# Kernel optimization log

Measured on AMD Instinct MI355X. Metric: run time of the kernel, lower is better.

The kernel has to match this reference:

```python
import jax, jax.numpy as jnp
import numpy as np

B, N, G, H, W = 2, 2000, 100, 800, 800
T = 200                      # TRAIN_ROIS_PER_IMAGE
POS_RATIO = 0.33
P = int(T * POS_RATIO)       # 66 positive ROIs
NEG = T - P                  # 134 negative ROIs
MH, MW = 28, 28              # MASK_SHAPE
BBOX_STD = jnp.array([0.1, 0.1, 0.2, 0.2], jnp.float32)


def _make_boxes(key, shape):
    # well-formed normalized boxes (y1,x1,y2,x2) with y1<y2, x1<x2
    k1, k2 = jax.random.split(key)
    y1x1 = jax.random.uniform(k1, shape + (2,)) * 0.7
    hw = 0.05 + jax.random.uniform(k2, shape + (2,)) * 0.25
    return jnp.concatenate([y1x1, y1x1 + hw], axis=-1)


def setup_inputs() -> dict:
    key = jax.random.key(0)
    k0, k1, k2, k3 = jax.random.split(key, 4)
    proposals = _make_boxes(k0, (B, N))
    gt_boxes = _make_boxes(k1, (B, G))
    gt_class_ids = jax.random.randint(k2, (B, G), 1, 81).astype(jnp.int32)
    gt_masks = jax.random.bernoulli(k3, 0.5, (B, H, W, G))
    return {"proposals": proposals, "gt_class_ids": gt_class_ids,
            "gt_boxes": gt_boxes, "gt_masks": gt_masks}


def _iou(b1, b2):
    # b1: [N,4], b2: [M,4] -> IoU [N,M]
    yy1 = jnp.maximum(b1[:, None, 0], b2[None, :, 0])
    xx1 = jnp.maximum(b1[:, None, 1], b2[None, :, 1])
    yy2 = jnp.minimum(b1[:, None, 2], b2[None, :, 2])
    xx2 = jnp.minimum(b1[:, None, 3], b2[None, :, 3])
    inter = jnp.clip(yy2 - yy1, 0, None) * jnp.clip(xx2 - xx1, 0, None)
    a1 = (b1[:, 2] - b1[:, 0]) * (b1[:, 3] - b1[:, 1])
    a2 = (b2[:, 2] - b2[:, 0]) * (b2[:, 3] - b2[:, 1])
    union = a1[:, None] + a2[None, :] - inter
    return inter / jnp.maximum(union, 1e-12)


def _refine(rois, gt):
    # box_refinement_graph: (dy, dx, log(dh), log(dw))
    h = rois[:, 2] - rois[:, 0]; w = rois[:, 3] - rois[:, 1]
    cy = rois[:, 0] + 0.5 * h;  cx = rois[:, 1] + 0.5 * w
    gh = gt[:, 2] - gt[:, 0];   gw = gt[:, 3] - gt[:, 1]
    gcy = gt[:, 0] + 0.5 * gh;  gcx = gt[:, 1] + 0.5 * gw
    return jnp.stack([(gcy - cy) / h, (gcx - cx) / w,
                      jnp.log(gh / h), jnp.log(gw / w)], axis=1)


def _crop_resize(img, box):
    # TF crop_and_resize (bilinear) of one [H,W] image to [MH,MW]
    by1, bx1, by2, bx2 = box[0], box[1], box[2], box[3]
    ys = by1 * (H - 1) + (jnp.arange(MH, dtype=img.dtype) / (MH - 1)) * (by2 - by1) * (H - 1)
    xs = bx1 * (W - 1) + (jnp.arange(MW, dtype=img.dtype) / (MW - 1)) * (bx2 - bx1) * (W - 1)
    y0f = jnp.floor(ys); x0f = jnp.floor(xs)
    wy = ys - y0f;       wx = xs - x0f
    y0 = jnp.clip(y0f.astype(jnp.int32), 0, H - 1); y1i = jnp.clip(y0 + 1, 0, H - 1)
    x0 = jnp.clip(x0f.astype(jnp.int32), 0, W - 1); x1i = jnp.clip(x0 + 1, 0, W - 1)
    v00 = img[y0[:, None], x0[None, :]]; v01 = img[y0[:, None], x1i[None, :]]
    v10 = img[y1i[:, None], x0[None, :]]; v11 = img[y1i[:, None], x1i[None, :]]
    top = v00 * (1 - wx)[None, :] + v01 * wx[None, :]
    bot = v10 * (1 - wx)[None, :] + v11 * wx[None, :]
    return top * (1 - wy)[:, None] + bot * wy[:, None]


def _per_image(props, cls, boxes, masks):
    overlaps = _iou(props, boxes)                    # [N, G]
    crowd = cls < 0
    ov = jnp.where(crowd[None, :], -1.0, overlaps)   # mask crowd GTs out
    roi_iou_max = ov.max(axis=1)
    crowd_max = jnp.where(crowd[None, :], overlaps, -1.0).max(axis=1)
    positive = roi_iou_max >= 0.5
    negative = (roi_iou_max < 0.5) & (crowd_max < 1e-3)
    # deterministic subsampling (top-IoU instead of TF random shuffle)
    _, pos_idx = jax.lax.top_k(jnp.where(positive, roi_iou_max, -1.0), P)
    pos_ok = positive[pos_idx]
    _, neg_idx = jax.lax.top_k(jnp.where(negative, roi_iou_max, -1.0), NEG)
    neg_ok = negative[neg_idx]

    pos_rois = props[pos_idx]                        # [P,4]
    assign = jnp.argmax(ov[pos_idx], axis=1)         # matched GT per positive
    roi_gt = boxes[assign]
    class_ids_pos = jnp.where(pos_ok, cls[assign], 0)
    deltas = jnp.where(pos_ok[:, None], _refine(pos_rois, roi_gt) / BBOX_STD, 0.0)

    mimg = jnp.transpose(masks, (2, 0, 1))[assign].astype(jnp.float32)  # [P,H,W]
    m = jax.vmap(_crop_resize)(mimg, pos_rois)       # [P,MH,MW]
    m = jnp.where(pos_ok[:, None, None], jnp.round(m), 0.0)

    rois = jnp.concatenate([jnp.where(pos_ok[:, None], pos_rois, 0.0),
                            jnp.where(neg_ok[:, None], props[neg_idx], 0.0)], axis=0)
    class_ids = jnp.concatenate([class_ids_pos, jnp.zeros((NEG,), jnp.int32)])
    deltas = jnp.concatenate([deltas, jnp.zeros((NEG, 4), deltas.dtype)])
    m = jnp.concatenate([m, jnp.zeros((NEG, MH, MW), m.dtype)])
    return rois, class_ids, deltas, m


def reference(proposals, gt_class_ids, gt_boxes, gt_masks):
    return jax.vmap(_per_image)(proposals, gt_class_ids, gt_boxes, gt_masks)
```

## Files before the change

kernel.cpp:

```cpp
#include <hip/hip_runtime.h>
#include <hip/hip_bf16.h>

#define BB 2
#define NN 2000
#define GG 100
#define HH 800
#define WW 800
#define TT 200
#define PP 66
#define NEGN 134
#define MHH 28
#define MWW 28

#define WS_IOU 0
#define WS_AMAX 16000
#define WS_FLAGS 32000
#define WS_POSIDX 48000
#define WS_NEGIDX 50048
#define WS_MODES 52096

enum { M_F32 = 0, M_BF16 = 1, M_I32 = 2, M_U8 = 3 };

__device__ __forceinline__ float bf16_to_f(unsigned short v) {
  return __uint_as_float(((unsigned int)v) << 16);
}

__device__ __forceinline__ float load_box_c(const void* p, long long elem, int mode) {
  if (mode == M_BF16) return bf16_to_f(((const unsigned short*)p)[elem]);
  return ((const float*)p)[elem];
}

__device__ __forceinline__ float load_mask(const void* p, size_t idx, int mode) {
  switch (mode) {
    case M_F32:  return ((const float*)p)[idx];
    case M_BF16: return ((const unsigned short*)p)[idx] ? 1.0f : 0.0f;
    case M_I32:  return ((const int*)p)[idx] ? 1.0f : 0.0f;
    default:     return ((const unsigned char*)p)[idx] ? 1.0f : 0.0f;
  }
}

__global__ void detect_modes(const unsigned int* props, const unsigned int* masks,
                             int* modes) {
  __shared__ int cnt[5];
  int tid = threadIdx.x;
  if (tid < 5) cnt[tid] = 0;
  __syncthreads();
  int lf = 0, lb = 0, li = 0, lu = 0, lbox = 0;
  for (int i = tid; i < 4096; i += 256) {
    unsigned int w = masks[i];
    if (w == 0u || w == 0x3F800000u) lf++;
    unsigned int lo = w & 0xFFFFu, hi = w >> 16;
    if ((lo == 0u || lo == 0x3F80u) && (hi == 0u || hi == 0x3F80u)) lb++;
    if (w <= 1u) li++;
    if ((w & 0xFEFEFEFEu) == 0u) lu++;
  }
  for (int i = tid; i < 4000; i += 256) {
    unsigned int w = props[i];
    float flo = bf16_to_f((unsigned short)(w & 0xFFFFu));
    float fhi = bf16_to_f((unsigned short)(w >> 16));
    if (flo >= 0.0f && flo <= 4.0f && fhi >= 0.0f && fhi <= 4.0f) lbox++;
  }
  atomicAdd(&cnt[0], lf); atomicAdd(&cnt[1], lb); atomicAdd(&cnt[2], li);
  atomicAdd(&cnt[3], lu); atomicAdd(&cnt[4], lbox);
  __syncthreads();
  if (tid == 0) {
    int mm;
    if (cnt[0] >= 4055) mm = M_F32;
    else if (cnt[1] >= 4055) mm = M_BF16;
    else if (cnt[2] >= 4055) mm = M_I32;
    else mm = M_U8;
    modes[0] = mm;
    modes[1] = (cnt[4] >= 2800) ? M_BF16 : M_F32;
  }
}

__global__ void iou_kernel(const void* props, const int* cls, const void* gtb,
                           const int* modes, float* iou_max, int* amax, int* flags) {
#pragma clang fp contract(off)
  int idx = blockIdx.x * blockDim.x + threadIdx.x;
  if (idx >= BB * NN) return;
  int bmode = modes[1];
  int b = idx / NN, i = idx - b * NN;
  long long e = (long long)(b * NN + i) * 4;
  float p0 = load_box_c(props, e + 0, bmode);
  float p1 = load_box_c(props, e + 1, bmode);
  float p2 = load_box_c(props, e + 2, bmode);
  float p3 = load_box_c(props, e + 3, bmode);
  float a1 = (p2 - p0) * (p3 - p1);
  float best = -1e30f; int bestg = 0; float crowdmax = -1.0f;
  for (int g = 0; g < GG; ++g) {
    long long ge = (long long)(b * GG + g) * 4;
    float g0 = load_box_c(gtb, ge + 0, bmode);
    float g1 = load_box_c(gtb, ge + 1, bmode);
    float g2 = load_box_c(gtb, ge + 2, bmode);
    float g3 = load_box_c(gtb, ge + 3, bmode);
    float yy1 = fmaxf(p0, g0), xx1 = fmaxf(p1, g1);
    float yy2 = fminf(p2, g2), xx2 = fminf(p3, g3);
    float ih = yy2 - yy1; if (ih < 0.0f) ih = 0.0f;
    float iw = xx2 - xx1; if (iw < 0.0f) iw = 0.0f;
    float inter = ih * iw;
    float a2 = (g2 - g0) * (g3 - g1);
    float uni = (a1 + a2) - inter;
    float iou = inter / fmaxf(uni, 1e-12f);
    bool crowd = cls[b * GG + g] < 0;
    float ov = crowd ? -1.0f : iou;
    if (ov > best) { best = ov; bestg = g; }
    float cv = crowd ? iou : -1.0f;
    if (cv > crowdmax) crowdmax = cv;
  }
  iou_max[idx] = best;
  amax[idx] = bestg;
  int f = 0;
  if (best >= 0.5f) f |= 1;
  if (best < 0.5f && crowdmax < 0.001f) f |= 2;
  flags[idx] = f;
}

__device__ __forceinline__ unsigned int ord_f32(float f) {
  unsigned int u = __float_as_uint(f);
  return (u & 0x80000000u) ? ~u : (u | 0x80000000u);
}

__global__ void __launch_bounds__(1024)
select_kernel(const float* iou, const int* flags, int* posidx, int* negidx) {
  __shared__ unsigned long long keys[2048];
  int b = blockIdx.x >> 1;
  int which = blockIdx.x & 1;
  int tid = threadIdx.x;
  for (int i = tid; i < 2048; i += 1024) {
    unsigned long long k = 0ull;
    if (i < NN) {
      int f = flags[b * NN + i];
      bool ok = which == 0 ? ((f & 1) != 0) : ((f & 2) != 0);
      float v = ok ? iou[b * NN + i] : -1.0f;
      k = (((unsigned long long)ord_f32(v)) << 32) | (unsigned long long)(2047 - i);
    }
    keys[i] = k;
  }
  __syncthreads();
  for (int kk = 2; kk <= 2048; kk <<= 1) {
    for (int j = kk >> 1; j > 0; j >>= 1) {
      for (int i = tid; i < 2048; i += 1024) {
        int ixj = i ^ j;
        if (ixj > i) {
          unsigned long long a = keys[i], c = keys[ixj];
          bool up = ((i & kk) == 0);
          if (up ? (a < c) : (a > c)) { keys[i] = c; keys[ixj] = a; }
        }
      }
      __syncthreads();
    }
  }
  int cnt = which == 0 ? PP : NEGN;
  int* dst = which == 0 ? (posidx + b * PP) : (negidx + b * NEGN);
  for (int t = tid; t < cnt; t += 1024)
    dst[t] = 2047 - (int)(keys[t] & 0xFFFFFFFFull);
}

__global__ void emit_kernel(const void* props, const int* cls, const void* gtb,
                            const int* modes, const int* flags, const int* amax,
                            const int* posidx, const int* negidx, float* out) {
#pragma clang fp contract(off)
  int id = blockIdx.x * blockDim.x + threadIdx.x;
  if (id >= BB * TT) return;
  int bmode = modes[1];
  int b = id / TT, t = id - b * TT;
  float r0 = 0, r1 = 0, r2 = 0, r3 = 0;
  float d0 = 0, d1 = 0, d2 = 0, d3 = 0;
  float cid = 0.0f;
  if (t < PP) {
    int i = posidx[b * PP + t];
    bool ok = (flags[b * NN + i] & 1) != 0;
    long long e = (long long)(b * NN + i) * 4;
    float p0 = load_box_c(props, e + 0, bmode), p1 = load_box_c(props, e + 1, bmode);
    float p2 = load_box_c(props, e + 2, bmode), p3 = load_box_c(props, e + 3, bmode);
    if (ok) {
      r0 = p0; r1 = p1; r2 = p2; r3 = p3;
      int g = amax[b * NN + i];
      cid = (float)cls[b * GG + g];
      long long ge = (long long)(b * GG + g) * 4;
      float g0 = load_box_c(gtb, ge + 0, bmode), g1 = load_box_c(gtb, ge + 1, bmode);
      float g2 = load_box_c(gtb, ge + 2, bmode), g3 = load_box_c(gtb, ge + 3, bmode);
      float h = p2 - p0, w = p3 - p1;
      float cy = p0 + 0.5f * h, cx = p1 + 0.5f * w;
      float gh = g2 - g0, gw = g3 - g1;
      float gcy = g0 + 0.5f * gh, gcx = g1 + 0.5f * gw;
      d0 = ((gcy - cy) / h) / 0.1f;
      d1 = ((gcx - cx) / w) / 0.1f;
      d2 = logf(gh / h) / 0.2f;
      d3 = logf(gw / w) / 0.2f;
    }
  } else {
    int j = negidx[b * NEGN + (t - PP)];
    bool ok = (flags[b * NN + j] & 2) != 0;
    if (ok) {
      long long e = (long long)(b * NN + j) * 4;
      r0 = load_box_c(props, e + 0, bmode); r1 = load_box_c(props, e + 1, bmode);
      r2 = load_box_c(props, e + 2, bmode); r3 = load_box_c(props, e + 3, bmode);
    }
  }
  int rb = (b * TT + t) * 4;
  out[rb + 0] = r0;
  out[rb + 1] = r1;
  out[rb + 2] = r2;
  out[rb + 3] = r3;
  out[1600 + b * TT + t] = cid;
  int db = 2000 + (b * TT + t) * 4;
  out[db + 0] = d0;
  out[db + 1] = d1;
  out[db + 2] = d2;
  out[db + 3] = d3;
}

__global__ void mask_kernel(const void* props, const void* gmask, const int* modes,
                            const int* flags, const int* amax, const int* posidx,
                            float* out) {
#pragma clang fp contract(off)
  int blk = blockIdx.x;
  int b = blk / TT, t = blk - b * TT;
  float* mout = out + 3600 + (size_t)blk * (MHH * MWW);
  bool ok = false; int g = 0;
  float by1 = 0, bx1 = 0, by2 = 0, bx2 = 0;
  if (t < PP) {
    int i = posidx[b * PP + t];
    ok = (flags[b * NN + i] & 1) != 0;
    g = amax[b * NN + i];
    int bmode = modes[1];
    long long e = (long long)(b * NN + i) * 4;
    by1 = load_box_c(props, e + 0, bmode); bx1 = load_box_c(props, e + 1, bmode);
    by2 = load_box_c(props, e + 2, bmode); bx2 = load_box_c(props, e + 3, bmode);
  }
  if (!ok) {
    for (int p = threadIdx.x; p < MHH * MWW; p += blockDim.x)
      mout[p] = 0.0f;
    return;
  }
  int mmode = modes[0];
  for (int p = threadIdx.x; p < MHH * MWW; p += blockDim.x) {
    int yy = p / MWW, xx = p - yy * MWW;
    float ty = (float)yy / 27.0f;
    float ys = by1 * 799.0f + (ty * (by2 - by1)) * 799.0f;
    float tx = (float)xx / 27.0f;
    float xs = bx1 * 799.0f + (tx * (bx2 - bx1)) * 799.0f;
    float y0f = floorf(ys), x0f = floorf(xs);
    float wy = ys - y0f, wx = xs - x0f;
    int y0 = (int)y0f; if (y0 < 0) y0 = 0; if (y0 > HH - 1) y0 = HH - 1;
    int y1 = y0 + 1;   if (y1 > HH - 1) y1 = HH - 1;
    int x0 = (int)x0f; if (x0 < 0) x0 = 0; if (x0 > WW - 1) x0 = WW - 1;
    int x1 = x0 + 1;   if (x1 > WW - 1) x1 = WW - 1;
    size_t rowb = (size_t)b * HH;
    size_t i00 = ((rowb + y0) * WW + x0) * GG + g;
    size_t i01 = ((rowb + y0) * WW + x1) * GG + g;
    size_t i10 = ((rowb + y1) * WW + x0) * GG + g;
    size_t i11 = ((rowb + y1) * WW + x1) * GG + g;
    float v00 = load_mask(gmask, i00, mmode);
    float v01 = load_mask(gmask, i01, mmode);
    float v10 = load_mask(gmask, i10, mmode);
    float v11 = load_mask(gmask, i11, mmode);
    float top = v00 * (1.0f - wx) + v01 * wx;
    float bot = v10 * (1.0f - wx) + v11 * wx;
    float m = top * (1.0f - wy) + bot * wy;
    m = rintf(m);
    mout[p] = m;
  }
}

extern "C" void kernel_launch(void* const* d_in, const int* in_sizes, int n_in,
                              void* d_out, int out_size, void* d_ws, size_t ws_size,
                              hipStream_t stream) {
  const void* props = d_in[0];
  const int* cls = (const int*)d_in[1];
  const void* gtb = d_in[2];
  const void* gmask = d_in[3];
  char* ws = (char*)d_ws;
  float* iou   = (float*)(ws + WS_IOU);
  int* amax    = (int*)(ws + WS_AMAX);
  int* flags   = (int*)(ws + WS_FLAGS);
  int* posidx  = (int*)(ws + WS_POSIDX);
  int* negidx  = (int*)(ws + WS_NEGIDX);
  int* modes   = (int*)(ws + WS_MODES);
  float* out = (float*)d_out;

  detect_modes<<<1, 256, 0, stream>>>((const unsigned int*)props,
                                      (const unsigned int*)gmask, modes);
  iou_kernel<<<(BB * NN + 255) / 256, 256, 0, stream>>>(props, cls, gtb, modes,
                                                        iou, amax, flags);
  select_kernel<<<BB * 2, 1024, 0, stream>>>(iou, flags, posidx, negidx);
  emit_kernel<<<(BB * TT + 255) / 256, 256, 0, stream>>>(props, cls, gtb, modes,
                                                         flags, amax, posidx, negidx, out);
  mask_kernel<<<BB * TT, 256, 0, stream>>>(props, gmask, modes, flags, amax, posidx, out);
}
```

Measured before the change: 651.9 us.

## Fuse mode detection, IoU, selection and emit into one per-image kernel

Merges the detect, IoU, bitonic-select and emit kernels into a single kernel with four blocks of 1024 threads. Each block recomputes the IoU for its image with GT boxes staged in shared memory, keeping IoU and flag data in shared memory instead of a global workspace. The mode-detection sample is reduced and uses wave ballots. This cuts launches and global round-trips, but the IoU work now runs on only 4 blocks (duplicated for the pos and neg halves), and the smaller detection sample could misclassify the input dtype.

Result: no change. 654.3 us (+0.4%).

```diff
diff --git a/kernel.cpp b/kernel.cpp
--- a/kernel.cpp
+++ b/kernel.cpp
@@ -1,5 +1,4 @@
 #include <hip/hip_runtime.h>
-#include <hip/hip_bf16.h>
 
 #define BB 2
 #define NN 2000
@@ -12,12 +11,9 @@
 #define MHH 28
 #define MWW 28
 
-#define WS_IOU 0
-#define WS_AMAX 16000
-#define WS_FLAGS 32000
-#define WS_POSIDX 48000
-#define WS_NEGIDX 50048
-#define WS_MODES 52096
+#define WS_BOX 0
+#define WS_OKG 2112
+#define WS_MODE 2644
 
 enum { M_F32 = 0, M_BF16 = 1, M_I32 = 2, M_U8 = 3 };
 
@@ -39,100 +35,102 @@
   }
 }
 
-__global__ void detect_modes(const unsigned int* props, const unsigned int* masks,
-                             int* modes) {
-  __shared__ int cnt[5];
-  int tid = threadIdx.x;
-  if (tid < 5) cnt[tid] = 0;
-  __syncthreads();
-  int lf = 0, lb = 0, li = 0, lu = 0, lbox = 0;
-  for (int i = tid; i < 4096; i += 256) {
-    unsigned int w = masks[i];
-    if (w == 0u || w == 0x3F800000u) lf++;
-    unsigned int lo = w & 0xFFFFu, hi = w >> 16;
-    if ((lo == 0u || lo == 0x3F80u) && (hi == 0u || hi == 0x3F80u)) lb++;
-    if (w <= 1u) li++;
-    if ((w & 0xFEFEFEFEu) == 0u) lu++;
-  }
-  for (int i = tid; i < 4000; i += 256) {
-    unsigned int w = props[i];
-    float flo = bf16_to_f((unsigned short)(w & 0xFFFFu));
-    float fhi = bf16_to_f((unsigned short)(w >> 16));
-    if (flo >= 0.0f && flo <= 4.0f && fhi >= 0.0f && fhi <= 4.0f) lbox++;
-  }
-  atomicAdd(&cnt[0], lf); atomicAdd(&cnt[1], lb); atomicAdd(&cnt[2], li);
-  atomicAdd(&cnt[3], lu); atomicAdd(&cnt[4], lbox);
-  __syncthreads();
-  if (tid == 0) {
-    int mm;
-    if (cnt[0] >= 4055) mm = M_F32;
-    else if (cnt[1] >= 4055) mm = M_BF16;
-    else if (cnt[2] >= 4055) mm = M_I32;
-    else mm = M_U8;
-    modes[0] = mm;
-    modes[1] = (cnt[4] >= 2800) ? M_BF16 : M_F32;
-  }
-}
-
-__global__ void iou_kernel(const void* props, const int* cls, const void* gtb,
-                           const int* modes, float* iou_max, int* amax, int* flags) {
-#pragma clang fp contract(off)
-  int idx = blockIdx.x * blockDim.x + threadIdx.x;
-  if (idx >= BB * NN) return;
-  int bmode = modes[1];
-  int b = idx / NN, i = idx - b * NN;
-  long long e = (long long)(b * NN + i) * 4;
-  float p0 = load_box_c(props, e + 0, bmode);
-  float p1 = load_box_c(props, e + 1, bmode);
-  float p2 = load_box_c(props, e + 2, bmode);
-  float p3 = load_box_c(props, e + 3, bmode);
-  float a1 = (p2 - p0) * (p3 - p1);
-  float best = -1e30f; int bestg = 0; float crowdmax = -1.0f;
-  for (int g = 0; g < GG; ++g) {
-    long long ge = (long long)(b * GG + g) * 4;
-    float g0 = load_box_c(gtb, ge + 0, bmode);
-    float g1 = load_box_c(gtb, ge + 1, bmode);
-    float g2 = load_box_c(gtb, ge + 2, bmode);
-    float g3 = load_box_c(gtb, ge + 3, bmode);
-    float yy1 = fmaxf(p0, g0), xx1 = fmaxf(p1, g1);
-    float yy2 = fminf(p2, g2), xx2 = fminf(p3, g3);
-    float ih = yy2 - yy1; if (ih < 0.0f) ih = 0.0f;
-    float iw = xx2 - xx1; if (iw < 0.0f) iw = 0.0f;
-    float inter = ih * iw;
-    float a2 = (g2 - g0) * (g3 - g1);
-    float uni = (a1 + a2) - inter;
-    float iou = inter / fmaxf(uni, 1e-12f);
-    bool crowd = cls[b * GG + g] < 0;
-    float ov = crowd ? -1.0f : iou;
-    if (ov > best) { best = ov; bestg = g; }
-    float cv = crowd ? iou : -1.0f;
-    if (cv > crowdmax) crowdmax = cv;
-  }
-  iou_max[idx] = best;
-  amax[idx] = bestg;
-  int f = 0;
-  if (best >= 0.5f) f |= 1;
-  if (best < 0.5f && crowdmax < 0.001f) f |= 2;
-  flags[idx] = f;
-}
-
 __device__ __forceinline__ unsigned int ord_f32(float f) {
   unsigned int u = __float_as_uint(f);
   return (u & 0x80000000u) ? ~u : (u | 0x80000000u);
 }
 
 __global__ void __launch_bounds__(1024)
-select_kernel(const float* iou, const int* flags, int* posidx, int* negidx) {
+fused_kernel(const void* props, const int* cls, const void* gtb,
+             const unsigned int* props_u, const unsigned int* masks_u,
+             float* out, float4* wbox, int* wokg, int* wmode) {
+#pragma clang fp contract(off)
+  __shared__ float gt0[GG], gt1[GG], gt2[GG], gt3[GG];
+  __shared__ int gcls[GG];
+  __shared__ float iouv[NN];
+  __shared__ int meta[NN];
   __shared__ unsigned long long keys[2048];
-  int b = blockIdx.x >> 1;
-  int which = blockIdx.x & 1;
+  __shared__ int cnt[4];
   int tid = threadIdx.x;
+  int b = blockIdx.x >> 1, which = blockIdx.x & 1;
+
+  if (tid < 4) cnt[tid] = 0;
+  __syncthreads();
+  {
+    unsigned int w = props_u[tid];
+    float flo = bf16_to_f((unsigned short)(w & 0xFFFFu));
+    float fhi = bf16_to_f((unsigned short)(w >> 16));
+    unsigned long long m = __ballot(flo >= 0.0f && flo <= 4.0f && fhi >= 0.0f && fhi <= 4.0f);
+    if ((tid & 63) == 0) atomicAdd(&cnt[0], __popcll(m));
+  }
+  if (blockIdx.x == 0) {
+    unsigned int w = masks_u[tid];
+    unsigned int lo = w & 0xFFFFu, hi = w >> 16;
+    unsigned long long m1 = __ballot(w == 0u || w == 0x3F800000u);
+    unsigned long long m2 = __ballot((lo == 0u || lo == 0x3F80u) && (hi == 0u || hi == 0x3F80u));
+    unsigned long long m3 = __ballot(w <= 1u);
+    if ((tid & 63) == 0) {
+      atomicAdd(&cnt[1], __popcll(m1));
+      atomicAdd(&cnt[2], __popcll(m2));
+      atomicAdd(&cnt[3], __popcll(m3));
+    }
+  }
+  __syncthreads();
+  int bmode = (cnt[0] >= 700) ? M_BF16 : M_F32;
+  if (blockIdx.x == 0 && tid == 0) {
+    int mm;
+    if (cnt[1] >= 1000) mm = M_F32;
+    else if (cnt[2] >= 1000) mm = M_BF16;
+    else if (cnt[3] >= 1000) mm = M_I32;
+    else mm = M_U8;
+    *wmode = mm;
+  }
+  if (tid < GG) {
+    long long ge = (long long)(b * GG + tid) * 4;
+    gt0[tid] = load_box_c(gtb, ge + 0, bmode);
+    gt1[tid] = load_box_c(gtb, ge + 1, bmode);
+    gt2[tid] = load_box_c(gtb, ge + 2, bmode);
+    gt3[tid] = load_box_c(gtb, ge + 3, bmode);
+    gcls[tid] = cls[b * GG + tid];
+  }
+  __syncthreads();
+  for (int i = tid; i < NN; i += 1024) {
+    long long e = (long long)(b * NN + i) * 4;
+    float p0 = load_box_c(props, e + 0, bmode);
+    float p1 = load_box_c(props, e + 1, bmode);
+    float p2 = load_box_c(props, e + 2, bmode);
+    float p3 = load_box_c(props, e + 3, bmode);
+    float a1 = (p2 - p0) * (p3 - p1);
+    float best = -1e30f; int bestg = 0; float crowdmax = -1.0f;
+    for (int g = 0; g < GG; ++g) {
+      float g0 = gt0[g], g1 = gt1[g], g2 = gt2[g], g3 = gt3[g];
+      float yy1 = fmaxf(p0, g0), xx1 = fmaxf(p1, g1);
+      float yy2 = fminf(p2, g2), xx2 = fminf(p3, g3);
+      float ih = yy2 - yy1; if (ih < 0.0f) ih = 0.0f;
+      float iw = xx2 - xx1; if (iw < 0.0f) iw = 0.0f;
+      float inter = ih * iw;
+      float a2 = (g2 - g0) * (g3 - g1);
+      float uni = (a1 + a2) - inter;
+      float iou = inter / fmaxf(uni, 1e-12f);
+      bool crowd = gcls[g] < 0;
+      float ov = crowd ? -1.0f : iou;
+      if (ov > best) { best = ov; bestg = g; }
+      float cv = crowd ? iou : -1.0f;
+      if (cv > crowdmax) crowdmax = cv;
+    }
+    int f = 0;
+    if (best >= 0.5f) f |= 1;
+    if (best < 0.5f && crowdmax < 0.001f) f |= 2;
+    iouv[i] = best;
+    meta[i] = (bestg << 2) | f;
+  }
+  __syncthreads();
   for (int i = tid; i < 2048; i += 1024) {
     unsigned long long k = 0ull;
     if (i < NN) {
-      int f = flags[b * NN + i];
-      bool ok = which == 0 ? ((f & 1) != 0) : ((f & 2) != 0);
-      float v = ok ? iou[b * NN + i] : -1.0f;
+      int m = meta[i];
+      bool ok = which == 0 ? ((m & 1) != 0) : ((m & 2) != 0);
+      float v = ok ? iouv[i] : -1.0f;
       k = (((unsigned long long)ord_f32(v)) << 32) | (unsigned long long)(2047 - i);
     }
     keys[i] = k;
@@ -151,91 +149,78 @@
       __syncthreads();
     }
   }
-  int cnt = which == 0 ? PP : NEGN;
-  int* dst = which == 0 ? (posidx + b * PP) : (negidx + b * NEGN);
-  for (int t = tid; t < cnt; t += 1024)
-    dst[t] = 2047 - (int)(keys[t] & 0xFFFFFFFFull);
-}
-
-__global__ void emit_kernel(const void* props, const int* cls, const void* gtb,
-                            const int* modes, const int* flags, const int* amax,
-                            const int* posidx, const int* negidx, float* out) {
-#pragma clang fp contract(off)
-  int id = blockIdx.x * blockDim.x + threadIdx.x;
-  if (id >= BB * TT) return;
-  int bmode = modes[1];
-  int b = id / TT, t = id - b * TT;
-  float r0 = 0, r1 = 0, r2 = 0, r3 = 0;
-  float d0 = 0, d1 = 0, d2 = 0, d3 = 0;
-  float cid = 0.0f;
-  if (t < PP) {
-    int i = posidx[b * PP + t];
-    bool ok = (flags[b * NN + i] & 1) != 0;
-    long long e = (long long)(b * NN + i) * 4;
-    float p0 = load_box_c(props, e + 0, bmode), p1 = load_box_c(props, e + 1, bmode);
-    float p2 = load_box_c(props, e + 2, bmode), p3 = load_box_c(props, e + 3, bmode);
-    if (ok) {
-      r0 = p0; r1 = p1; r2 = p2; r3 = p3;
-      int g = amax[b * NN + i];
-      cid = (float)cls[b * GG + g];
-      long long ge = (long long)(b * GG + g) * 4;
-      float g0 = load_box_c(gtb, ge + 0, bmode), g1 = load_box_c(gtb, ge + 1, bmode);
-      float g2 = load_box_c(gtb, ge + 2, bmode), g3 = load_box_c(gtb, ge + 3, bmode);
-      float h = p2 - p0, w = p3 - p1;
-      float cy = p0 + 0.5f * h, cx = p1 + 0.5f * w;
-      float gh = g2 - g0, gw = g3 - g1;
-      float gcy = g0 + 0.5f * gh, gcx = g1 + 0.5f * gw;
-      d0 = ((gcy - cy) / h) / 0.1f;
-      d1 = ((gcx - cx) / w) / 0.1f;
-      d2 = logf(gh / h) / 0.2f;
-      d3 = logf(gw / w) / 0.2f;
+  if (which == 0) {
+    if (tid < PP) {
+      int i = 2047 - (int)(keys[tid] & 0xFFFFFFFFull);
+      int m = meta[i];
+      int ok = m & 1;
+      int g = m >> 2;
+      long long e = (long long)(b * NN + i) * 4;
+      float p0 = load_box_c(props, e + 0, bmode), p1 = load_box_c(props, e + 1, bmode);
+      float p2 = load_box_c(props, e + 2, bmode), p3 = load_box_c(props, e + 3, bmode);
+      float r0 = 0, r1 = 0, r2 = 0, r3 = 0, d0 = 0, d1 = 0, d2 = 0, d3 = 0, cid = 0.0f;
+      if (ok) {
+        r0 = p0; r1 = p1; r2 = p2; r3 = p3;
+        cid = (float)gcls[g];
+        float h = p2 - p0, w = p3 - p1;
+        float cy = p0 + 0.5f * h, cx = p1 + 0.5f * w;
+        float gh = gt2[g] - gt0[g], gw = gt3[g] - gt1[g];
+        float gcy = gt0[g] + 0.5f * gh, gcx = gt1[g] + 0.5f * gw;
+        d0 = ((gcy - cy) / h) / 0.1f;
+        d1 = ((gcx - cx) / w) / 0.1f;
+        d2 = logf(gh / h) / 0.2f;
+        d3 = logf(gw / w) / 0.2f;
+      }
+      int row = b * TT + tid;
+      int rb = row * 4;
+      out[rb + 0] = r0; out[rb + 1] = r1; out[rb + 2] = r2; out[rb + 3] = r3;
+      out[1600 + row] = cid;
+      int db = 2000 + row * 4;
+      out[db + 0] = d0; out[db + 1] = d1; out[db + 2] = d2; out[db + 3] = d3;
+      wbox[b * PP + tid] = make_float4(p0, p1, p2, p3);
+      wokg[b * PP + tid] = (g << 1) | ok;
     }
   } else {
-    int j = negidx[b * NEGN + (t - PP)];
-    bool ok = (flags[b * NN + j] & 2) != 0;
-    if (ok) {
-      long long e = (long long)(b * NN + j) * 4;
-      r0 = load_box_c(props, e + 0, bmode); r1 = load_box_c(props, e + 1, bmode);
-      r2 = load_box_c(props, e + 2, bmode); r3 = load_box_c(props, e + 3, bmode);
-    }
-  }
-  int rb = (b * TT + t) * 4;
-  out[rb + 0] = r0;
-  out[rb + 1] = r1;
-  out[rb + 2] = r2;
-  out[rb + 3] = r3;
-  out[1600 + b * TT + t] = cid;
-  int db = 2000 + (b * TT + t) * 4;
-  out[db + 0] = d0;
-  out[db + 1] = d1;
-  out[db + 2] = d2;
-  out[db + 3] = d3;
-}
-
-__global__ void mask_kernel(const void* props, const void* gmask, const int* modes,
-                            const int* flags, const int* amax, const int* posidx,
-                            float* out) {
+    if (tid < NEGN) {
+      int j = 2047 - (int)(keys[tid] & 0xFFFFFFFFull);
+      int ok = (meta[j] >> 1) & 1;
+      float r0 = 0, r1 = 0, r2 = 0, r3 = 0;
+      if (ok) {
+        long long e = (long long)(b * NN + j) * 4;
+        r0 = load_box_c(props, e + 0, bmode); r1 = load_box_c(props, e + 1, bmode);
+        r2 = load_box_c(props, e + 2, bmode); r3 = load_box_c(props, e + 3, bmode);
+      }
+      int row = b * TT + PP + tid;
+      int rb = row * 4;
+      out[rb + 0] = r0; out[rb + 1] = r1; out[rb + 2] = r2; out[rb + 3] = r3;
+      out[1600 + row] = 0.0f;
+      int db = 2000 + row * 4;
+      out[db + 0] = 0.0f; out[db + 1] = 0.0f; out[db + 2] = 0.0f; out[db + 3] = 0.0f;
+    }
+  }
+}
+
+__global__ void mask_kernel(const void* gmask, const float4* wbox, const int* wokg,
+                            const int* wmode, float* out) {
 #pragma clang fp contract(off)
   int blk = blockIdx.x;
   int b = blk / TT, t = blk - b * TT;
   float* mout = out + 3600 + (size_t)blk * (MHH * MWW);
-  bool ok = false; int g = 0;
+  int ok = 0, g = 0;
   float by1 = 0, bx1 = 0, by2 = 0, bx2 = 0;
   if (t < PP) {
-    int i = posidx[b * PP + t];
-    ok = (flags[b * NN + i] & 1) != 0;
-    g = amax[b * NN + i];
-    int bmode = modes[1];
-    long long e = (long long)(b * NN + i) * 4;
-    by1 = load_box_c(props, e + 0, bmode); bx1 = load_box_c(props, e + 1, bmode);
-    by2 = load_box_c(props, e + 2, bmode); bx2 = load_box_c(props, e + 3, bmode);
+    int og = wokg[b * PP + t];
+    ok = og & 1;
+    g = og >> 1;
+    float4 bx = wbox[b * PP + t];
+    by1 = bx.x; bx1 = bx.y; by2 = bx.z; bx2 = bx.w;
   }
   if (!ok) {
     for (int p = threadIdx.x; p < MHH * MWW; p += blockDim.x)
       mout[p] = 0.0f;
     return;
   }
-  int mmode = modes[0];
+  int mmode = *wmode;
   for (int p = threadIdx.x; p < MHH * MWW; p += blockDim.x) {
     int yy = p / MWW, xx = p - yy * MWW;
     float ty = (float)yy / 27.0f;
@@ -273,20 +258,14 @@
   const void* gtb = d_in[2];
   const void* gmask = d_in[3];
   char* ws = (char*)d_ws;
-  float* iou   = (float*)(ws + WS_IOU);
-  int* amax    = (int*)(ws + WS_AMAX);
-  int* flags   = (int*)(ws + WS_FLAGS);
-  int* posidx  = (int*)(ws + WS_POSIDX);
-  int* negidx  = (int*)(ws + WS_NEGIDX);
-  int* modes   = (int*)(ws + WS_MODES);
+  float4* wbox = (float4*)(ws + WS_BOX);
+  int* wokg    = (int*)(ws + WS_OKG);
+  int* wmode   = (int*)(ws + WS_MODE);
   float* out = (float*)d_out;
 
-  detect_modes<<<1, 256, 0, stream>>>((const unsigned int*)props,
-                                      (const unsigned int*)gmask, modes);
-  iou_kernel<<<(BB * NN + 255) / 256, 256, 0, stream>>>(props, cls, gtb, modes,
-                                                        iou, amax, flags);
-  select_kernel<<<BB * 2, 1024, 0, stream>>>(iou, flags, posidx, negidx);
-  emit_kernel<<<(BB * TT + 255) / 256, 256, 0, stream>>>(props, cls, gtb, modes,
-                                                         flags, amax, posidx, negidx, out);
-  mask_kernel<<<BB * TT, 256, 0, stream>>>(props, gmask, modes, flags, amax, posidx, out);
-}
+  fused_kernel<<<BB * 2, 1024, 0, stream>>>(props, cls, gtb,
+                                            (const unsigned int*)props,
+                                            (const unsigned int*)gmask,
+                                            out, wbox, wokg, wmode);
+  mask_kernel<<<BB * TT, 256, 0, stream>>>(gmask, wbox, wokg, wmode, out);
+}
```
